# Optimization experiments

Hardware: AMD Instinct MI355X
Metric: run time of the kernel (lower is better)

## Reference

```python
import jax, jax.numpy as jnp
import numpy as np
from jax import lax


def setup_inputs() -> dict:
    key = jax.random.key(0)
    k1, k2 = jax.random.split(key)
    B, T, TAG = 128, 512, 256  # TAG = tagset_size + 2
    in_features = jax.random.normal(k1, (B, T, TAG), dtype=jnp.float32)
    mask = jnp.ones((B, T), dtype=jnp.int32)
    transitions = jax.random.normal(k2, (TAG, TAG), dtype=jnp.float32) * 0.1
    return {"in_features": in_features, "mask": mask, "transitions": transitions}


def _viterbi(in_features, transitions, mask):
    # Faithful NCRF++-style CRF viterbi decode.
    # scores[t, b, f, to] = emission[t, b, to] + transitions[f, to]
    B, T, TAG = in_features.shape
    START, STOP = TAG - 2, TAG - 1
    lengths = jnp.sum(mask, axis=1).astype(jnp.int32)            # (B,)
    featsT = jnp.transpose(in_features, (1, 0, 2))               # (T, B, TAG)
    maskT = jnp.transpose(mask, (1, 0))                          # (T, B)

    # initial partition: row START of scores at t=0
    part0 = featsT[0] + transitions[START][None, :]              # (B, TAG)

    def step(partition, inp):
        emit, m = inp                                            # (B,TAG), (B,)
        cur = emit[:, None, :] + transitions[None] + partition[:, :, None]  # (B, from, to)
        new_part = jnp.max(cur, axis=1)                          # (B, TAG)
        bp = jnp.argmax(cur, axis=1).astype(jnp.int32)           # (B, TAG)
        bp = jnp.where(m[:, None] > 0, bp, 0)                    # mask backpointers to 0
        return new_part, (new_part, bp)

    _, (parts, bps) = lax.scan(step, part0, (featsT[1:], maskT[1:]))
    part_hist = jnp.concatenate([part0[None], parts], axis=0)    # (T, B, TAG)

    last_idx = lengths - 1                                       # (B,)
    last_partition = jnp.take_along_axis(
        jnp.transpose(part_hist, (1, 0, 2)), last_idx[:, None, None], axis=1
    )[:, 0]                                                      # (B, TAG)

    # transition to any last tag, pick STOP column
    last_values = last_partition[:, :, None] + transitions[None]  # (B, from, to)
    path_vals = jnp.max(last_values, axis=1)                     # (B, TAG)
    last_bp = jnp.argmax(last_values, axis=1).astype(jnp.int32)  # (B, TAG)
    path_score = path_vals[:, STOP][:, None]                     # (B, 1)
    pointer = last_bp[:, STOP]                                   # (B,)

    # backpointer sequence: [bp_1 .. bp_{T-1}, pad]; insert final pointer at last valid pos
    pad = jnp.zeros((1, B, TAG), dtype=jnp.int32)
    bp_seq = jnp.concatenate([bps, pad], axis=0)                 # (T, B, TAG)
    bp_seq = jnp.transpose(bp_seq, (1, 0, 2))                    # (B, T, TAG)
    bp_seq = bp_seq.at[jnp.arange(B), last_idx, :].set(pointer[:, None])
    bp_seq = jnp.transpose(bp_seq, (1, 0, 2))                    # (T, B, TAG)

    def back_step(ptr, bp_t):
        new_ptr = jnp.take_along_axis(bp_t, ptr[:, None], axis=1)[:, 0]
        return new_ptr, new_ptr

    _, ptrs = lax.scan(back_step, pointer, bp_seq[:-1], reverse=True)  # (T-1, B)
    decode_idx = jnp.concatenate([ptrs, pointer[None]], axis=0)  # (T, B)
    return path_score, jnp.transpose(decode_idx, (1, 0))         # (B,1), (B,T)


def reference(in_features, mask, transitions):
    return _viterbi(in_features, transitions, mask)
```

## Files before the change

kernel.cpp:

```cpp
#include <hip/hip_runtime.h>

#define NB 128
#define TT 512
#define TAG 256
#define START (TAG - 2)
#define STOP (TAG - 1)
#define MARGIN 0.03125f
#define NSLOT 8

__global__ __launch_bounds__(64) void viterbi_wave(
    const float* __restrict__ feats,
    const int*   __restrict__ mask,
    const float* __restrict__ trans,
    float* __restrict__ out)
{
    __shared__ unsigned int bp2[TT][64];
    __shared__ float pcand[TAG];
    __shared__ int   cand[TAG];
    __shared__ float dec_s[TT];

    const int b    = blockIdx.x;
    const int lane = threadIdx.x;

    const float* __restrict__ fb = feats + (size_t)b * TT * TAG;
    const int*   __restrict__ mb = mask  + (size_t)b * TT;

    int lm = 0;
    #pragma unroll
    for (int k = 0; k < 8; ++k) lm += mb[(k << 6) + lane];
    #pragma unroll
    for (int o = 32; o; o >>= 1) lm += __shfl_xor(lm, o);
    const int lastidx = (lm > 0) ? (lm - 1) : 0;

    float tmx = -INFINITY, tmn = INFINITY;
    #pragma unroll 8
    for (int k = lane; k < TAG * TAG / 4; k += 64) {
        float4 v = ((const float4*)trans)[k];
        tmx = fmaxf(tmx, fmaxf(fmaxf(v.x, v.y), fmaxf(v.z, v.w)));
        tmn = fminf(tmn, fminf(fminf(v.x, v.y), fminf(v.z, v.w)));
    }
    #pragma unroll
    for (int o = 32; o; o >>= 1) {
        tmx = fmaxf(tmx, __shfl_xor(tmx, o));
        tmn = fminf(tmn, __shfl_xor(tmn, o));
    }
    const float Wwin = (tmx - tmn) + MARGIN;

    float m[4], pl[4];
    #pragma unroll
    for (int s = 0; s < 4; ++s) {
        const int j = (s << 6) + lane;
        m[s]  = fb[j] + trans[START * TAG + j];
        pl[s] = m[s];
    }

    float eA[4], eB[4];
    #pragma unroll
    for (int s = 0; s < 4; ++s) eA[s] = fb[TAG + (s << 6) + lane];
    #pragma unroll
    for (int s = 0; s < 4; ++s) eB[s] = fb[2 * TAG + (s << 6) + lane];
    int mkA = mb[1];
    int mkB = mb[2];

    for (int t = 1; t < TT; ++t) {
        float e0[4];
        #pragma unroll
        for (int s = 0; s < 4; ++s) e0[s] = eA[s];
        const int mk = mkA;
        #pragma unroll
        for (int s = 0; s < 4; ++s) eA[s] = eB[s];
        mkA = mkB;
        const int tp = (t + 2 <= TT - 1) ? (t + 2) : (TT - 1);
        #pragma unroll
        for (int s = 0; s < 4; ++s) eB[s] = fb[(size_t)tp * TAG + (s << 6) + lane];
        mkB = mb[tp];

        float px = fmaxf(fmaxf(m[0], m[1]), fmaxf(m[2], m[3]));
        #pragma unroll
        for (int o = 32; o; o >>= 1) px = fmaxf(px, __shfl_xor(px, o));
        const float thr = px - Wwin;

        const unsigned long long bal0 = __ballot(m[0] >= thr);
        const unsigned long long bal1 = __ballot(m[1] >= thr);
        const unsigned long long bal2 = __ballot(m[2] >= thr);
        const unsigned long long bal3 = __ballot(m[3] >= thr);
        const int c0 = __popcll(bal0), c1 = __popcll(bal1),
                  c2 = __popcll(bal2), c3 = __popcll(bal3);
        const unsigned long long below = (1ull << lane) - 1ull;
        if (m[0] >= thr) { int r =                __popcll(bal0 & below); cand[r] = lane;       pcand[r] = m[0]; }
        if (m[1] >= thr) { int r = c0 +           __popcll(bal1 & below); cand[r] = 64  + lane; pcand[r] = m[1]; }
        if (m[2] >= thr) { int r = c0 + c1 +      __popcll(bal2 & below); cand[r] = 128 + lane; pcand[r] = m[2]; }
        if (m[3] >= thr) { int r = c0 + c1 + c2 + __popcll(bal3 & below); cand[r] = 192 + lane; pcand[r] = m[3]; }
        const int ncand = c0 + c1 + c2 + c3;

        float nm[4];
        int   bi[4];
        #pragma unroll
        for (int c = 0; c < 4; ++c) { nm[c] = -INFINITY; bi[c] = 0; }

        int   ics[NSLOT];
        float pvs[NSLOT];
        #pragma unroll
        for (int k = 0; k < NSLOT; ++k) {
            const int   icr = cand[k];
            const float pvr = pcand[k];
            const bool  ok  = (k < ncand);
            ics[k] = ok ? icr : 0;
            pvs[k] = ok ? pvr : -INFINITY;
        }
        float tv[NSLOT][4];
        #pragma unroll
        for (int k = 0; k < NSLOT; ++k) {
            #pragma unroll
            for (int c = 0; c < 4; ++c)
                tv[k][c] = trans[(size_t)ics[k] * TAG + (c << 6) + lane];
        }
        #pragma unroll
        for (int k = 0; k < NSLOT; ++k) {
            #pragma unroll
            for (int c = 0; c < 4; ++c) {
                const float cur = (e0[c] + tv[k][c]) + pvs[k];
                if (cur > nm[c]) { nm[c] = cur; bi[c] = ics[k]; }
            }
        }
        for (int k = NSLOT; k < ncand; ++k) {
            const int   icr = cand[k];
            const float pvr = pcand[k];
            #pragma unroll
            for (int c = 0; c < 4; ++c) {
                const float cur = (e0[c] + trans[(size_t)icr * TAG + (c << 6) + lane]) + pvr;
                if (cur > nm[c]) { nm[c] = cur; bi[c] = icr; }
            }
        }

        const unsigned int pack = (unsigned)bi[0] | ((unsigned)bi[1] << 8)
                                | ((unsigned)bi[2] << 16) | ((unsigned)bi[3] << 24);
        bp2[t][lane] = (mk > 0) ? pack : 0u;

        #pragma unroll
        for (int c = 0; c < 4; ++c) m[c] = nm[c];
        if (t == lastidx) {
            #pragma unroll
            for (int c = 0; c < 4; ++c) pl[c] = nm[c];
        }
    }

    float bv; int bj;
    {
        const float fv0 = pl[0] + trans[(size_t)lane         * TAG + STOP];
        const float fv1 = pl[1] + trans[(size_t)(64  + lane) * TAG + STOP];
        const float fv2 = pl[2] + trans[(size_t)(128 + lane) * TAG + STOP];
        const float fv3 = pl[3] + trans[(size_t)(192 + lane) * TAG + STOP];
        bv = fv0; bj = lane;
        if (fv1 > bv) { bv = fv1; bj = 64  + lane; }
        if (fv2 > bv) { bv = fv2; bj = 128 + lane; }
        if (fv3 > bv) { bv = fv3; bj = 192 + lane; }
        #pragma unroll
        for (int o = 32; o; o >>= 1) {
            const float ov = __shfl_xor(bv, o);
            const int   oj = __shfl_xor(bj, o);
            if (ov > bv || (ov == bv && oj < bj)) { bv = ov; bj = oj; }
        }
    }

    if (lane == 0) {
        out[b] = bv;
        int cur = bj;
        dec_s[TT - 1] = (float)cur;
        const unsigned char* bpb = (const unsigned char*)bp2;
        for (int s = TT - 2; s >= 0; --s) {
            cur = (s == lastidx) ? bj
                                 : (int)bpb[((s + 1) << 8) + ((cur & 63) << 2) + (cur >> 6)];
            dec_s[s] = (float)cur;
        }
    }

    float* dec = out + NB + (size_t)b * TT;
    #pragma unroll
    for (int k = 0; k < 8; ++k) dec[(k << 6) + lane] = dec_s[(k << 6) + lane];
}

extern "C" void kernel_launch(void* const* d_in, const int* in_sizes, int n_in,
                              void* d_out, int out_size, void* d_ws, size_t ws_size,
                              hipStream_t stream) {
    const float* feats = (const float*)d_in[0];
    const int*   mask  = (const int*)d_in[1];
    const float* trans = (const float*)d_in[2];
    float* out = (float*)d_out;
    viterbi_wave<<<NB, 64, 0, stream>>>(feats, mask, trans, out);
}
```

Baseline: 918.1 us.

## Use DPP max reduction, scalar candidate indices, and tree combine in viterbi step

Replaces the shuffle-based wave max with DPP row operations plus a readlane, and makes the candidate indices wave-uniform via readfirstlane so transition rows are addressed through scalar registers. The serial per-candidate compare chain becomes a pairwise tree reduction, and candidates beyond the first slots are handled by a second batch of eight before falling back to a loop. The next-step emission prefetch moves after the transition loads, and the candidate buffers are zero-initialised so unused slots hold valid indices. The aim is to shorten the latency of the serial per-timestep critical path. Tree tie-breaking may pick a different index than the sequential first-max rule when scores are equal.

```diff
diff --git a/kernel.cpp b/kernel.cpp
--- a/kernel.cpp
+++ b/kernel.cpp
@@ -7,6 +7,15 @@
 #define STOP (TAG - 1)
 #define MARGIN 0.03125f
 #define NSLOT 8
+
+#define DPPMAX(x, ctrl) do {                                                   \
+    float _t = __int_as_float(__builtin_amdgcn_update_dpp(                     \
+        __float_as_int(x), __float_as_int(x), (ctrl), 0xf, 0xf, false));       \
+    (x) = fmaxf((x), _t); } while (0)
+
+#define COMB(va, ia, vb, ib) do {                                              \
+    const bool _g = ((vb) > (va));                                             \
+    (va) = _g ? (vb) : (va); (ia) = _g ? (ib) : (ia); } while (0)
 
 __global__ __launch_bounds__(64) void viterbi_wave(
     const float* __restrict__ feats,
@@ -25,12 +34,25 @@
     const float* __restrict__ fb = feats + (size_t)b * TT * TAG;
     const int*   __restrict__ mb = mask  + (size_t)b * TT;
 
+    float e00[4], eA[4], eB[4];
+    #pragma unroll
+    for (int s = 0; s < 4; ++s) e00[s] = fb[(s << 6) + lane];
+    #pragma unroll
+    for (int s = 0; s < 4; ++s) eA[s] = fb[TAG + (s << 6) + lane];
+    #pragma unroll
+    for (int s = 0; s < 4; ++s) eB[s] = fb[2 * TAG + (s << 6) + lane];
+
+    #pragma unroll
+    for (int s = 0; s < 4; ++s) { cand[(s << 6) + lane] = 0; pcand[(s << 6) + lane] = -INFINITY; }
+
     int lm = 0;
     #pragma unroll
     for (int k = 0; k < 8; ++k) lm += mb[(k << 6) + lane];
     #pragma unroll
     for (int o = 32; o; o >>= 1) lm += __shfl_xor(lm, o);
     const int lastidx = (lm > 0) ? (lm - 1) : 0;
+    int mkA = mb[1];
+    int mkB = mb[2];
 
     float tmx = -INFINITY, tmn = INFINITY;
     #pragma unroll 8
@@ -49,18 +71,9 @@
     float m[4], pl[4];
     #pragma unroll
     for (int s = 0; s < 4; ++s) {
-        const int j = (s << 6) + lane;
-        m[s]  = fb[j] + trans[START * TAG + j];
+        m[s]  = e00[s] + trans[START * TAG + (s << 6) + lane];
         pl[s] = m[s];
     }
-
-    float eA[4], eB[4];
-    #pragma unroll
-    for (int s = 0; s < 4; ++s) eA[s] = fb[TAG + (s << 6) + lane];
-    #pragma unroll
-    for (int s = 0; s < 4; ++s) eB[s] = fb[2 * TAG + (s << 6) + lane];
-    int mkA = mb[1];
-    int mkB = mb[2];
 
     for (int t = 1; t < TT; ++t) {
         float e0[4];
@@ -70,15 +83,17 @@
         #pragma unroll
         for (int s = 0; s < 4; ++s) eA[s] = eB[s];
         mkA = mkB;
-        const int tp = (t + 2 <= TT - 1) ? (t + 2) : (TT - 1);
-        #pragma unroll
-        for (int s = 0; s < 4; ++s) eB[s] = fb[(size_t)tp * TAG + (s << 6) + lane];
-        mkB = mb[tp];
-
-        float px = fmaxf(fmaxf(m[0], m[1]), fmaxf(m[2], m[3]));
-        #pragma unroll
-        for (int o = 32; o; o >>= 1) px = fmaxf(px, __shfl_xor(px, o));
-        const float thr = px - Wwin;
+
+        float red = fmaxf(fmaxf(m[0], m[1]), fmaxf(m[2], m[3]));
+        DPPMAX(red, 0x111);
+        DPPMAX(red, 0x112);
+        DPPMAX(red, 0x114);
+        DPPMAX(red, 0x118);
+        DPPMAX(red, 0x142);
+        DPPMAX(red, 0x143);
+        const float pmax = __int_as_float(
+            __builtin_amdgcn_readlane(__float_as_int(red), 63));
+        const float thr = pmax - Wwin;
 
         const unsigned long long bal0 = __ballot(m[0] >= thr);
         const unsigned long long bal1 = __ballot(m[1] >= thr);
@@ -93,43 +108,83 @@
         if (m[3] >= thr) { int r = c0 + c1 + c2 + __popcll(bal3 & below); cand[r] = 192 + lane; pcand[r] = m[3]; }
         const int ncand = c0 + c1 + c2 + c3;
 
+        int   ics[NSLOT];
+        float pvs[NSLOT];
+        #pragma unroll
+        for (int k = 0; k < NSLOT; ++k) {
+            ics[k] = __builtin_amdgcn_readfirstlane(cand[k]) & 255;
+            pvs[k] = (k < ncand) ? pcand[k] : -INFINITY;
+        }
+        float tv[NSLOT][4];
+        #pragma unroll
+        for (int k = 0; k < NSLOT; ++k) {
+            const float* tb = trans + ((size_t)ics[k] << 8);
+            #pragma unroll
+            for (int c = 0; c < 4; ++c) tv[k][c] = tb[lane + (c << 6)];
+        }
+        const int tp = (t + 2 <= TT - 1) ? (t + 2) : (TT - 1);
+        #pragma unroll
+        for (int s = 0; s < 4; ++s) eB[s] = fb[(size_t)tp * TAG + (s << 6) + lane];
+        mkB = mb[tp];
+
         float nm[4];
         int   bi[4];
         #pragma unroll
-        for (int c = 0; c < 4; ++c) { nm[c] = -INFINITY; bi[c] = 0; }
-
-        int   ics[NSLOT];
-        float pvs[NSLOT];
-        #pragma unroll
-        for (int k = 0; k < NSLOT; ++k) {
-            const int   icr = cand[k];
-            const float pvr = pcand[k];
-            const bool  ok  = (k < ncand);
-            ics[k] = ok ? icr : 0;
-            pvs[k] = ok ? pvr : -INFINITY;
-        }
-        float tv[NSLOT][4];
-        #pragma unroll
-        for (int k = 0; k < NSLOT; ++k) {
-            #pragma unroll
-            for (int c = 0; c < 4; ++c)
-                tv[k][c] = trans[(size_t)ics[k] * TAG + (c << 6) + lane];
-        }
-        #pragma unroll
-        for (int k = 0; k < NSLOT; ++k) {
+        for (int c = 0; c < 4; ++c) {
+            float cv[NSLOT]; int ci[NSLOT];
+            #pragma unroll
+            for (int k = 0; k < NSLOT; ++k) {
+                cv[k] = (e0[c] + tv[k][c]) + pvs[k];
+                ci[k] = ics[k];
+            }
+            #pragma unroll
+            for (int st = 1; st < NSLOT; st <<= 1)
+                #pragma unroll
+                for (int k = 0; k + st < NSLOT; k += (st << 1))
+                    COMB(cv[k], ci[k], cv[k + st], ci[k + st]);
+            nm[c] = cv[0];
+            bi[c] = ci[0];
+        }
+
+        if (ncand > NSLOT) {
+            int   ics2[NSLOT];
+            float pvs2[NSLOT];
+            #pragma unroll
+            for (int k = 0; k < NSLOT; ++k) {
+                ics2[k] = __builtin_amdgcn_readfirstlane(cand[NSLOT + k]) & 255;
+                pvs2[k] = (NSLOT + k < ncand) ? pcand[NSLOT + k] : -INFINITY;
+            }
+            float tv2[NSLOT][4];
+            #pragma unroll
+            for (int k = 0; k < NSLOT; ++k) {
+                const float* tb = trans + ((size_t)ics2[k] << 8);
+                #pragma unroll
+                for (int c = 0; c < 4; ++c) tv2[k][c] = tb[lane + (c << 6)];
+            }
             #pragma unroll
             for (int c = 0; c < 4; ++c) {
-                const float cur = (e0[c] + tv[k][c]) + pvs[k];
-                if (cur > nm[c]) { nm[c] = cur; bi[c] = ics[k]; }
-            }
-        }
-        for (int k = NSLOT; k < ncand; ++k) {
-            const int   icr = cand[k];
-            const float pvr = pcand[k];
-            #pragma unroll
-            for (int c = 0; c < 4; ++c) {
-                const float cur = (e0[c] + trans[(size_t)icr * TAG + (c << 6) + lane]) + pvr;
-                if (cur > nm[c]) { nm[c] = cur; bi[c] = icr; }
+                float cv[NSLOT]; int ci[NSLOT];
+                #pragma unroll
+                for (int k = 0; k < NSLOT; ++k) {
+                    cv[k] = (e0[c] + tv2[k][c]) + pvs2[k];
+                    ci[k] = ics2[k];
+                }
+                #pragma unroll
+                for (int st = 1; st < NSLOT; st <<= 1)
+                    #pragma unroll
+                    for (int k = 0; k + st < NSLOT; k += (st << 1))
+                        COMB(cv[k], ci[k], cv[k + st], ci[k + st]);
+                COMB(nm[c], bi[c], cv[0], ci[0]);
+            }
+            for (int k = 2 * NSLOT; k < ncand; ++k) {
+                const int   icr = __builtin_amdgcn_readfirstlane(cand[k]) & 255;
+                const float pvr = pcand[k];
+                const float* tb = trans + ((size_t)icr << 8);
+                #pragma unroll
+                for (int c = 0; c < 4; ++c) {
+                    const float cur = (e0[c] + tb[lane + (c << 6)]) + pvr;
+                    COMB(nm[c], bi[c], cur, icr);
+                }
             }
         }
 
```

Result: slower. 1.264 ms (+37.7%).
